# Optimization experiments

Hardware: AMD Instinct MI355X
Metric: run time of the kernel (lower is better)

## Reference

```python
import jax, jax.numpy as jnp
import numpy as np

NUM_CLASSES = 80
STRIDES = (8, 16, 32)
FEAT_HW = ((80, 80), (40, 40), (20, 20))
B = 32
MAX_GT = 60


def setup_inputs() -> dict:
    key = jax.random.key(0)
    ks = jax.random.split(key, 6)
    feats = {}
    for i, (s, (h, w)) in enumerate(zip(STRIDES, FEAT_HW)):
        feats[f"feat{s}"] = jax.random.normal(ks[i], (B, 5 + NUM_CLASSES, h, w), jnp.float32)
    u = jax.random.uniform(ks[3], (B, MAX_GT, 4), jnp.float32)
    # cx,cy in [0,640), w,h in [8,128): realistic pixel-space gt boxes for a 640x640 image
    gt_boxes = jnp.concatenate([u[..., :2] * 640.0, u[..., 2:] * 120.0 + 8.0], -1)
    gt_classes = jax.random.randint(ks[4], (B, MAX_GT), 0, NUM_CLASSES)
    num_gts = jax.random.randint(ks[5], (B,), 1, MAX_GT + 1)
    return dict(feat8=feats["feat8"], feat16=feats["feat16"], feat32=feats["feat32"],
                gt_boxes=gt_boxes, gt_classes=gt_classes, num_gts=num_gts)


def _decode(feat, stride):
    # torch get_output_and_grid: xy=(raw+grid)*stride, wh=exp(raw)*stride
    b, c, h, w = feat.shape
    yv, xv = jnp.meshgrid(jnp.arange(h), jnp.arange(w), indexing="ij")
    gx = xv.reshape(-1).astype(feat.dtype)  # [H*W]
    gy = yv.reshape(-1).astype(feat.dtype)
    out = feat.reshape(b, c, h * w).transpose(0, 2, 1)  # [B,A,C]
    xy = (out[..., :2] + jnp.stack([gx, gy], -1)[None]) * stride
    wh = jnp.exp(out[..., 2:4]) * stride
    return jnp.concatenate([xy, wh, out[..., 4:]], -1), gx, gy


def _pair_iou(a, b):
    # a: [G,4] xywh, b: [A,4] xywh -> [G,A] IoU (bboxes_iou, xyxy=False)
    tl = jnp.maximum(a[:, None, :2] - a[:, None, 2:] * 0.5, b[None, :, :2] - b[None, :, 2:] * 0.5)
    br = jnp.minimum(a[:, None, :2] + a[:, None, 2:] * 0.5, b[None, :, :2] + b[None, :, 2:] * 0.5)
    en = jnp.all(tl < br, -1)
    inter = jnp.where(en, jnp.prod(br - tl, -1), 0.0)
    area_a = jnp.prod(a[:, 2:], -1)
    area_b = jnp.prod(b[:, 2:], -1)
    return inter / (area_a[:, None] + area_b[None, :] - inter + 1e-16)


def _bce_logits(x, t):
    return jnp.maximum(x, 0.0) - x * t + jnp.log1p(jnp.exp(-jnp.abs(x)))


def _iou_loss(pred, tgt):
    # IOUloss(loss_type='iou'): 1 - iou^2, per box
    tl = jnp.maximum(pred[..., :2] - pred[..., 2:] * 0.5, tgt[..., :2] - tgt[..., 2:] * 0.5)
    br = jnp.minimum(pred[..., :2] + pred[..., 2:] * 0.5, tgt[..., :2] + tgt[..., 2:] * 0.5)
    en = jnp.all(tl < br, -1)
    inter = jnp.where(en, jnp.prod(br - tl, -1), 0.0)
    union = jnp.prod(pred[..., 2:], -1) + jnp.prod(tgt[..., 2:], -1) - inter
    iou = inter / (union + 1e-16)
    return 1.0 - iou ** 2


def _assign(boxes, cls_lo, obj_lo, gtb, gtc, vmask, cx, cy, st):
    # SimOTA per image. boxes [A,4], cls_lo [A,C], obj_lo [A], gtb [G,4], gtc [G] int,
    # vmask [G] bool (gt padding), cx/cy/st [A] anchor centers & strides.
    G, A = gtb.shape[0], boxes.shape[0]
    iou = _pair_iou(gtb, boxes)  # [G,A]
    gx, gy = gtb[:, :1], gtb[:, 1:2]
    gw, gh = gtb[:, 2:3], gtb[:, 3:4]
    in_box = ((cx[None] > gx - 0.5 * gw) & (cx[None] < gx + 0.5 * gw) &
              (cy[None] > gy - 0.5 * gh) & (cy[None] < gy + 0.5 * gh))
    R = 2.5  # center sampling radius (in strides)
    in_ctr = ((cx[None] > gx - R * st[None]) & (cx[None] < gx + R * st[None]) &
              (cy[None] > gy - R * st[None]) & (cy[None] < gy + R * st[None]))
    fg = ((in_box | in_ctr) & vmask[:, None]).any(0)  # [A] candidate anchors
    in_both = (in_box & in_ctr).astype(boxes.dtype)
    # pairwise cls cost: BCE(sqrt(sig(cls)*sig(obj)), onehot(gt_cls)).sum(-1),
    # decomposed to avoid the [G,A,C] tensor: sum_c bce0 + (bce1-bce0)[gt_cls]
    p = jnp.clip(jnp.sqrt(jax.nn.sigmoid(cls_lo) * jax.nn.sigmoid(obj_lo)[:, None]), 1e-7, 1.0 - 1e-7)
    bce1 = -jnp.log(p)          # [A,C]
    bce0 = -jnp.log(1.0 - p)    # [A,C]
    cls_cost = bce0.sum(-1)[None, :] + (bce1 - bce0)[:, gtc].T  # [G,A]
    cost = (cls_cost + 3.0 * (-jnp.log(iou + 1e-8))
            + 100000.0 * (1.0 - in_both)
            + 1e9 * (~fg)[None, :].astype(boxes.dtype)
            + 1e9 * (~vmask)[:, None].astype(boxes.dtype))
    K = 10  # n_candidate_k
    topk_ious, _ = jax.lax.top_k(iou * fg[None, :], K)
    dyn_k = jnp.maximum(topk_ious.sum(-1).astype(jnp.int32), 1)  # clamp(int(sum), min=1)
    _, pos = jax.lax.top_k(-cost, K)  # [G,K] lowest-cost anchors per gt
    sel = (jnp.arange(K)[None, :] < dyn_k[:, None]).astype(boxes.dtype)
    matching = jnp.zeros((G, A), boxes.dtype).at[jnp.arange(G)[:, None], pos].set(sel)
    matching = matching * vmask[:, None].astype(boxes.dtype)
    # resolve anchors claimed by >1 gt: keep min-cost gt
    conflict = matching.sum(0) > 1
    best_gt = jnp.argmin(cost, axis=0)  # [A]
    matching = jnp.where(conflict[None, :], jax.nn.one_hot(best_gt, G, dtype=matching.dtype).T, matching)
    fg_final = matching.sum(0) > 0  # [A]
    matched = jnp.argmax(matching, axis=0)  # [A]
    pred_iou = (matching * iou).sum(0)  # [A]
    cls_t = jax.nn.one_hot(gtc[matched], NUM_CLASSES, dtype=boxes.dtype) * pred_iou[:, None]
    reg_t = gtb[matched]
    return fg_final, cls_t, reg_t


def _forward(feat8, feat16, feat32, gt_boxes, gt_classes, num_gts):
    outs, cxs, cys, sts = [], [], [], []
    for f, s in zip((feat8, feat16, feat32), STRIDES):
        o, gx, gy = _decode(f, float(s))
        outs.append(o)
        cxs.append((gx + 0.5) * s)
        cys.append((gy + 0.5) * s)
        sts.append(jnp.full_like(gx, s))
    preds = jnp.concatenate(outs, 1)  # [B,A,5+C]
    cx = jnp.concatenate(cxs)
    cy = jnp.concatenate(cys)
    st = jnp.concatenate(sts)
    boxes = preds[..., :4]
    obj_lo = preds[..., 4]
    cls_lo = preds[..., 5:]
    vmask = jnp.arange(MAX_GT)[None, :] < num_gts[:, None]
    fg, cls_t, reg_t = jax.vmap(_assign, in_axes=(0, 0, 0, 0, 0, 0, None, None, None))(
        boxes, cls_lo, obj_lo, gt_boxes, gt_classes, vmask, cx, cy, st)
    # SimOTA assignment is no_grad in YOLOX: targets are constants wrt preds
    fg = jax.lax.stop_gradient(fg)
    cls_t = jax.lax.stop_gradient(cls_t)
    reg_t = jax.lax.stop_gradient(reg_t)
    fg_f = fg.astype(boxes.dtype)
    num_fg = jnp.maximum(fg_f.sum(), 1.0)
    loss_iou = (_iou_loss(boxes, reg_t) * fg_f).sum()
    loss_obj = _bce_logits(obj_lo, fg_f * 0.9).sum()  # obj_targets * 0.9 smoothing
    loss_cls = (_bce_logits(cls_lo, cls_t) * fg_f[..., None]).sum()
    REG_WEIGHT = 5.0
    return (REG_WEIGHT * loss_iou + loss_obj + loss_cls) / num_fg


def reference(feat8, feat16, feat32, gt_boxes, gt_classes, num_gts):
    return _forward(feat8, feat16, feat32, gt_boxes, gt_classes, num_gts)
```

## Files before the change

kernel.cpp:

```cpp
#include <hip/hip_runtime.h>

constexpr int kB = 32;
constexpr int kA = 8400;
constexpr int kG = 60;
constexpr int kC = 80;
constexpr int kK = 10;
constexpr int kNBx = (kA + 255)/256;
constexpr int kNB = kNBx * kB;

__device__ __forceinline__ float fexp(float x){ return __expf(x); }
__device__ __forceinline__ float flog(float x){ return __logf(x); }
__device__ __forceinline__ float frcp(float x){ return __builtin_amdgcn_rcpf(x); }
__device__ __forceinline__ float frsq(float x){ return __builtin_amdgcn_rsqf(x); }
__device__ __forceinline__ float fsqrt(float x){ return __builtin_amdgcn_sqrtf(x); }
__device__ __forceinline__ float fdiv(float a, float b){ return a * __builtin_amdgcn_rcpf(b); }
__device__ __forceinline__ float sigm(float x){ return frcp(1.0f + fexp(-x)); }
__device__ __forceinline__ float bce(float x, float t){
  return fmaxf(x, 0.0f) - x*t + flog(1.0f + fexp(-fabsf(x)));
}

__device__ __forceinline__ unsigned ordbits(float v){
  unsigned u = __float_as_uint(v);
  return (u & 0x80000000u) ? ~u : (u | 0x80000000u);
}
__device__ __forceinline__ float unpackf(unsigned k){
  return __uint_as_float((k & 0x80000000u) ? (k & 0x7fffffffu) : ~k);
}

struct AInfo { int x, y; float st; };
__device__ __forceinline__ AInfo ainfo(int a){
  AInfo r;
  if (a < 6400)      { r.x = a % 80;           r.y = a / 80;           r.st = 8.0f;  }
  else if (a < 8000) { int l = a-6400; r.x = l % 40; r.y = l / 40;     r.st = 16.0f; }
  else               { int l = a-8000; r.x = l % 20; r.y = l / 20;     r.st = 32.0f; }
  return r;
}

__device__ __forceinline__ float featv(const float* __restrict__ f8,
                                       const float* __restrict__ f16,
                                       const float* __restrict__ f32x,
                                       int b, int ch, int a){
  if (a < 6400) return f8 [(b*85 + ch)*6400 + a];
  if (a < 8000) return f16[(b*85 + ch)*1600 + (a - 6400)];
  return             f32x[(b*85 + ch)*400  + (a - 8000)];
}

__device__ __forceinline__ float pair_iou(float4 g, float4 p){
  float tlx = fmaxf(g.x - g.z*0.5f, p.x - p.z*0.5f);
  float tly = fmaxf(g.y - g.w*0.5f, p.y - p.w*0.5f);
  float brx = fminf(g.x + g.z*0.5f, p.x + p.z*0.5f);
  float bry = fminf(g.y + g.w*0.5f, p.y + p.w*0.5f);
  float inter = (tlx < brx && tly < bry) ? (brx-tlx)*(bry-tly) : 0.0f;
  return fdiv(inter, g.z*g.w + p.z*p.w - inter + 1e-16f);
}

__device__ __forceinline__ float cost_core(float iou, float cl, float obs, float b0sum,
                                           int a, float4 gt, int fg_a){
  AInfo ai = ainfo(a);
  float cx = ((float)ai.x + 0.5f)*ai.st;
  float cy = ((float)ai.y + 0.5f)*ai.st;
  bool in_box = (cx > gt.x - 0.5f*gt.z) && (cx < gt.x + 0.5f*gt.z)
             && (cy > gt.y - 0.5f*gt.w) && (cy < gt.y + 0.5f*gt.w);
  bool in_ctr = (cx > gt.x - 2.5f*ai.st) && (cx < gt.x + 2.5f*ai.st)
             && (cy > gt.y - 2.5f*ai.st) && (cy < gt.y + 2.5f*ai.st);
  float p = fsqrt(sigm(cl) * obs);
  p = fminf(fmaxf(p, 1e-7f), 1.0f - 1e-7f);
  float diff = -flog(p) + flog(1.0f - p);
  float c = b0sum + diff;
  c += 3.0f * (-flog(iou + 1e-8f));
  c += (in_box && in_ctr) ? 0.0f : 100000.0f;
  c += fg_a ? 0.0f : 1000000000.0f;
  return c;
}

__device__ __forceinline__ void insert10(unsigned long long* arr, unsigned long long key){
  if (key > arr[kK-1]){
    arr[kK-1] = key;
    #pragma unroll
    for (int i = kK-1; i > 0; --i)
      if (arr[i] > arr[i-1]){ unsigned long long t = arr[i]; arr[i] = arr[i-1]; arr[i-1] = t; }
  }
}

__global__ __launch_bounds__(256) void k_decode(
    const float* __restrict__ f8, const float* __restrict__ f16, const float* __restrict__ f32x,
    const float* __restrict__ gtb, const int* __restrict__ ngts,
    float* __restrict__ boxes, float* __restrict__ objl, float* __restrict__ b0s,
    float* __restrict__ bceS, float* __restrict__ obsA,
    int* __restrict__ fg, int* __restrict__ cnt, int* __restrict__ mtch){
  int b = blockIdx.y;
  int tid = threadIdx.x;
  int a = blockIdx.x*256 + tid;
  __shared__ float4 sg[kG];
  if (tid < kG) sg[tid] = ((const float4*)gtb)[b*kG + tid];
  __syncthreads();
  if (a >= kA) return;
  int ng = ngts[b];
  const float* base; int hw, off; float st_; int gx, gy;
  if (a < 6400)      { base=f8;   hw=6400; off=a;        st_=8.0f;  gx=off%80; gy=off/80; }
  else if (a < 8000) { base=f16;  hw=1600; off=a-6400;   st_=16.0f; gx=off%40; gy=off/40; }
  else               { base=f32x; hw=400;  off=a-8000;   st_=32.0f; gx=off%20; gy=off/20; }
  const float* p0 = base + ((size_t)b*85)*hw + off;
  float t0 = p0[0];
  float t1 = p0[(size_t)hw];
  float t2 = p0[(size_t)2*hw];
  float t3 = p0[(size_t)3*hw];
  float ob = p0[(size_t)4*hw];
  float4 bx;
  bx.x = (t0 + (float)gx) * st_;
  bx.y = (t1 + (float)gy) * st_;
  bx.z = fexp(t2) * st_;
  bx.w = fexp(t3) * st_;
  int idx = b*kA + a;
  ((float4*)boxes)[idx] = bx;
  objl[idx] = ob;
  float obs = sigm(ob);
  obsA[idx] = obs;
  float so = fsqrt(obs);
  float s = 0.0f;
  float sumCl = 0.0f;
  float slogv = 0.0f;
  const float* pc = p0 + (size_t)5*hw;
  #pragma unroll 2
  for (int grp = 0; grp < kC/8; ++grp){
    float prodS = 1.0f, prodV = 1.0f;
    #pragma unroll
    for (int j = 0; j < 8; ++j){
      float cl = pc[(size_t)(grp*8 + j)*hw];
      float u = fexp(-cl);
      float v = 1.0f + u;
      float p = so * frsq(v);
      p = fminf(fmaxf(p, 1e-7f), 1.0f - 1e-7f);
      prodS *= (1.0f - p);
      prodV *= v;
      sumCl += cl;
    }
    s -= flog(prodS);
    slogv += flog(prodV);
  }
  b0s[idx] = s;
  bceS[idx] = sumCl + slogv;
  float cx = ((float)gx + 0.5f)*st_;
  float cy = ((float)gy + 0.5f)*st_;
  int f = 0;
  for (int g = 0; g < ng; ++g){
    float4 gt = sg[g];
    bool in_box = (cx > gt.x - 0.5f*gt.z) && (cx < gt.x + 0.5f*gt.z)
               && (cy > gt.y - 0.5f*gt.w) && (cy < gt.y + 0.5f*gt.w);
    bool in_ctr = (cx > gt.x - 2.5f*st_) && (cx < gt.x + 2.5f*st_)
               && (cy > gt.y - 2.5f*st_) && (cy < gt.y + 2.5f*st_);
    if (in_box || in_ctr){ f = 1; break; }
  }
  fg[idx] = f;
  cnt[idx] = 0;
  mtch[idx] = 0x7fffffff;
}

__global__ __launch_bounds__(1024) void k_compact(
    const int* __restrict__ fg, unsigned short* __restrict__ alist, int* __restrict__ mcnt){
  int b = blockIdx.x;
  int tid = threadIdx.x;
  const int CH = 9;
  int start = tid*CH;
  int myf[CH]; int cl = 0;
  #pragma unroll
  for (int j = 0; j < CH; ++j){
    int a = start + j;
    int f = (a < kA) ? fg[b*kA + a] : 0;
    myf[j] = f; cl += f;
  }
  __shared__ int s1[1024], s2[1024];
  int* cur = s1; int* nxt = s2;
  cur[tid] = cl; __syncthreads();
  for (int off = 1; off < 1024; off <<= 1){
    int v = cur[tid];
    if (tid >= off) v += cur[tid - off];
    nxt[tid] = v; __syncthreads();
    int* t = cur; cur = nxt; nxt = t;
  }
  int o = cur[tid] - cl;
  unsigned short* out = alist + (size_t)b*kA;
  #pragma unroll
  for (int j = 0; j < CH; ++j){
    int a = start + j;
    if (a < kA && myf[j]) out[o++] = (unsigned short)a;
  }
  if (tid == 1023) mcnt[b] = cur[tid];
}

__global__ __launch_bounds__(256) void k_assign(
    const float* __restrict__ f8, const float* __restrict__ f16, const float* __restrict__ f32x,
    const float* __restrict__ gtb, const int* __restrict__ gtc, const int* __restrict__ ngts,
    const float* __restrict__ boxes, const float* __restrict__ obsA, const float* __restrict__ b0s,
    const int* __restrict__ fg, const unsigned short* __restrict__ alist, const int* __restrict__ mcnt,
    int* __restrict__ cnt, int* __restrict__ mtch){
  int b = blockIdx.x / kG;
  int g = blockIdx.x % kG;
  if (g >= ngts[b]) return;
  int tid = threadIdx.x;
  int lane = tid & 63, wid = tid >> 6;
  float4 gt = ((const float4*)gtb)[b*kG + g];
  int cls = gtc[b*kG + g];
  const float4* bx4 = (const float4*)boxes;
  const float* c8  = f8   + ((size_t)b*85 + 5 + cls)*6400;
  const float* c16 = f16  + ((size_t)b*85 + 5 + cls)*1600;
  const float* c32 = f32x + ((size_t)b*85 + 5 + cls)*400;
  int m = mcnt[b];
  bool full0 = (m < kK);
  int len = full0 ? kA : m;
  const unsigned short* al = alist + (size_t)b*kA;

  __shared__ unsigned long long stop1[4][kK], stop2[4][kK];
  __shared__ int swb[4];

  unsigned long long k1[kK], k2[kK];
  #pragma unroll
  for (int i = 0; i < kK; ++i){ k1[i] = 0ull; k2[i] = 0ull; }
  int nboth = 0;

  for (int i = tid; i < len; i += 256){
    int a = full0 ? i : (int)al[i];
    int idx = b*kA + a;
    float4 bx = bx4[idx];
    float iou = pair_iou(gt, bx);
    if (full0){
      int fga = fg[idx];
      float v = fga ? iou : 0.0f;
      insert10(k1, ((unsigned long long)ordbits(v) << 32) | (unsigned)(~a));
      float cl = (a < 6400) ? c8[a] : (a < 8000) ? c16[a-6400] : c32[a-8000];
      float c = cost_core(iou, cl, obsA[idx], b0s[idx], a, gt, fga);
      insert10(k2, ~(((unsigned long long)ordbits(c) << 32) | (unsigned)a));
    } else {
      insert10(k1, ((unsigned long long)ordbits(iou) << 32) | (unsigned)(~a));
      AInfo ai = ainfo(a);
      float cx = ((float)ai.x + 0.5f)*ai.st;
      float cy = ((float)ai.y + 0.5f)*ai.st;
      bool in_box = (cx > gt.x - 0.5f*gt.z) && (cx < gt.x + 0.5f*gt.z)
                 && (cy > gt.y - 0.5f*gt.w) && (cy < gt.y + 0.5f*gt.w);
      bool in_ctr = (cx > gt.x - 2.5f*ai.st) && (cx < gt.x + 2.5f*ai.st)
                 && (cy > gt.y - 2.5f*ai.st) && (cy < gt.y + 2.5f*ai.st);
      if (in_box && in_ctr){
        ++nboth;
        float cl = (a < 6400) ? c8[a] : (a < 8000) ? c16[a-6400] : c32[a-8000];
        float c = cost_core(iou, cl, obsA[idx], b0s[idx], a, gt, 1);
        insert10(k2, ~(((unsigned long long)ordbits(c) << 32) | (unsigned)a));
      }
    }
  }

  int nb = nboth;
  #pragma unroll
  for (int off = 32; off; off >>= 1) nb += __shfl_down(nb, off, 64);
  if (lane == 0) swb[wid] = nb;
  __syncthreads();
  int sboth = swb[0] + swb[1] + swb[2] + swb[3];

  if (!full0 && sboth < kK){
    #pragma unroll
    for (int i = 0; i < kK; ++i) k2[i] = 0ull;
    for (int i = tid; i < len; i += 256){
      int a = (int)al[i];
      int idx = b*kA + a;
      float iou = pair_iou(gt, bx4[idx]);
      float cl = (a < 6400) ? c8[a] : (a < 8000) ? c16[a-6400] : c32[a-8000];
      float c = cost_core(iou, cl, obsA[idx], b0s[idx], a, gt, 1);
      insert10(k2, ~(((unsigned long long)ordbits(c) << 32) | (unsigned)a));
    }
  }

  #pragma unroll 1
  for (int k = 0; k < kK; ++k){
    unsigned long long best = k1[0];
    #pragma unroll
    for (int off = 32; off; off >>= 1){
      unsigned long long o = __shfl_xor(best, off, 64);
      if (o > best) best = o;
    }
    if (k1[0] == best){
      #pragma unroll
      for (int i = 0; i < kK-1; ++i) k1[i] = k1[i+1];
      k1[kK-1] = 0ull;
    }
    if (lane == 0) stop1[wid][k] = best;
  }
  #pragma unroll 1
  for (int k = 0; k < kK; ++k){
    unsigned long long best = k2[0];
    #pragma unroll
    for (int off = 32; off; off >>= 1){
      unsigned long long o = __shfl_xor(best, off, 64);
      if (o > best) best = o;
    }
    if (k2[0] == best){
      #pragma unroll
      for (int i = 0; i < kK-1; ++i) k2[i] = k2[i+1];
      k2[kK-1] = 0ull;
    }
    if (lane == 0) stop2[wid][k] = best;
  }
  __syncthreads();

  if (wid == 0){
    unsigned long long cand1 = (lane < 40) ? stop1[lane/kK][lane % kK] : 0ull;
    unsigned long long cand2 = (lane < 40) ? stop2[lane/kK][lane % kK] : 0ull;
    float ksum = 0.0f;
    #pragma unroll 1
    for (int k = 0; k < kK; ++k){
      unsigned long long best = cand1;
      #pragma unroll
      for (int off = 32; off; off >>= 1){
        unsigned long long o = __shfl_xor(best, off, 64);
        if (o > best) best = o;
      }
      if (cand1 == best) cand1 = 0ull;
      ksum += unpackf((unsigned)(best >> 32));
    }
    int dynk = max((int)ksum, 1);
    int my_a = -1;
    #pragma unroll 1
    for (int k = 0; k < kK; ++k){
      unsigned long long best = cand2;
      #pragma unroll
      for (int off = 32; off; off >>= 1){
        unsigned long long o = __shfl_xor(best, off, 64);
        if (o > best) best = o;
      }
      if (cand2 == best) cand2 = 0ull;
      if (lane == k) my_a = (int)((unsigned)(~best) & 0xffffffffu);
    }
    if (lane < kK && lane < dynk){
      atomicAdd(&cnt[b*kA + my_a], 1);
      atomicMin(&mtch[b*kA + my_a], g);
    }
  }
}

__global__ __launch_bounds__(256) void k_loss(
    const float* __restrict__ f8, const float* __restrict__ f16, const float* __restrict__ f32x,
    const float* __restrict__ gtb, const int* __restrict__ gtc, const int* __restrict__ ngts,
    const float* __restrict__ boxes, const float* __restrict__ objl, const float* __restrict__ b0s,
    const float* __restrict__ bceS, const float* __restrict__ obsA,
    const int* __restrict__ fg, const int* __restrict__ cnt, const int* __restrict__ mtch,
    float4* __restrict__ pacc){
  int b = blockIdx.y;
  int a = blockIdx.x*256 + threadIdx.x;
  int tid = threadIdx.x;
  __shared__ float4 sg[kG];
  __shared__ int scls[kG];
  if (tid < kG){ sg[tid] = ((const float4*)gtb)[b*kG + tid]; scls[tid] = gtc[b*kG + tid]; }
  __syncthreads();
  float li = 0.0f, lo = 0.0f, lc = 0.0f, nf = 0.0f;
  bool valid = (a < kA);
  int idx = valid ? (b*kA + a) : (b*kA);
  int c = valid ? cnt[idx] : 0;
  float ob = valid ? objl[idx] : 0.0f;
  float4 bx = valid ? ((const float4*)boxes)[idx] : make_float4(0,0,1,1);

  float fgf = 0.0f; int mg = 0;
  if (valid && c == 1){ mg = mtch[idx]; fgf = 1.0f; }
  bool need = valid && (c > 1);
  if (__any(need)){
    if (need){
      int ng = ngts[b];
      float b0 = b0s[idx];
      float obs = obsA[idx];
      int fga = fg[idx];
      float bestc = 3.0e38f; int bg = 0;
      for (int g = 0; g < ng; ++g){
        float iou = pair_iou(sg[g], bx);
        float cl = featv(f8,f16,f32x,b,5+scls[g],a);
        float cst = cost_core(iou, cl, obs, b0, a, sg[g], fga);
        if (cst < bestc){ bestc = cst; bg = g; }
      }
      mg = bg; fgf = 1.0f;
    }
  }
  if (valid){
    lo = bce(ob, fgf*0.9f);
    if (fgf > 0.0f){
      nf = 1.0f;
      float4 r = sg[mg];
      float piou = pair_iou(r, bx);
      float tlx = fmaxf(bx.x - bx.z*0.5f, r.x - r.z*0.5f);
      float tly = fmaxf(bx.y - bx.w*0.5f, r.y - r.w*0.5f);
      float brx = fminf(bx.x + bx.z*0.5f, r.x + r.z*0.5f);
      float bry = fminf(bx.y + bx.w*0.5f, r.y + r.w*0.5f);
      float inter = (tlx < brx && tly < bry) ? (brx-tlx)*(bry-tly) : 0.0f;
      float un = bx.z*bx.w + r.z*r.w - inter;
      float iou = fdiv(inter, un + 1e-16f);
      li = 1.0f - iou*iou;
      int tc = scls[mg];
      float cl_tc = featv(f8,f16,f32x,b,5+tc,a);
      lc = bceS[idx] - piou * cl_tc;
    }
  }
  for (int off = 32; off > 0; off >>= 1){
    li += __shfl_down(li, off, 64);
    lo += __shfl_down(lo, off, 64);
    lc += __shfl_down(lc, off, 64);
    nf += __shfl_down(nf, off, 64);
  }
  __shared__ float4 wred[4];
  int wid = tid >> 6;
  if ((tid & 63) == 0) wred[wid] = make_float4(li, lo, lc, nf);
  __syncthreads();
  if (tid == 0){
    float4 t = wred[0];
    for (int w = 1; w < 4; ++w){
      float4 o = wred[w];
      t.x += o.x; t.y += o.y; t.z += o.z; t.w += o.w;
    }
    pacc[blockIdx.y * gridDim.x + blockIdx.x] = t;
  }
}

__global__ __launch_bounds__(256) void k_final(
    const float4* __restrict__ pacc, float* __restrict__ out){
  int tid = threadIdx.x;
  float li = 0.0f, lo = 0.0f, lc = 0.0f, nf = 0.0f;
  for (int i = tid; i < kNB; i += 256){
    float4 p = pacc[i];
    li += p.x; lo += p.y; lc += p.z; nf += p.w;
  }
  for (int off = 32; off > 0; off >>= 1){
    li += __shfl_down(li, off, 64);
    lo += __shfl_down(lo, off, 64);
    lc += __shfl_down(lc, off, 64);
    nf += __shfl_down(nf, off, 64);
  }
  __shared__ float4 wred[4];
  int wid = tid >> 6;
  if ((tid & 63) == 0) wred[wid] = make_float4(li, lo, lc, nf);
  __syncthreads();
  if (tid == 0){
    float4 t = wred[0];
    for (int w = 1; w < 4; ++w){
      float4 o = wred[w];
      t.x += o.x; t.y += o.y; t.z += o.z; t.w += o.w;
    }
    out[0] = (5.0f*t.x + t.y + t.z) * frcp(fmaxf(t.w, 1.0f));
  }
}

extern "C" void kernel_launch(void* const* d_in, const int* in_sizes, int n_in,
                              void* d_out, int out_size, void* d_ws, size_t ws_size,
                              hipStream_t stream) {
  (void)in_sizes; (void)n_in; (void)out_size; (void)ws_size;
  const float* f8   = (const float*)d_in[0];
  const float* f16  = (const float*)d_in[1];
  const float* f32x = (const float*)d_in[2];
  const float* gtb  = (const float*)d_in[3];
  const int*   gtc  = (const int*)d_in[4];
  const int*   ngts = (const int*)d_in[5];
  float* out = (float*)d_out;

  const size_t BA = (size_t)kB*kA;
  float* ws    = (float*)d_ws;
  float* boxes = ws;
  float* objl  = boxes + BA*4;
  float* b0s   = objl  + BA;
  float* bceS  = b0s   + BA;
  float* obsA  = bceS  + BA;
  int*   fg    = (int*)(obsA + BA);
  int*   cnt   = fg  + BA;
  int*   mtch  = cnt + BA;
  unsigned short* alist = (unsigned short*)(mtch + BA);
  int*   mcnt  = (int*)(alist + BA);
  float4* pacc = (float4*)(mcnt + kB);

  dim3 gBA(kNBx, kB);
  k_decode<<<gBA, dim3(256), 0, stream>>>(f8,f16,f32x,gtb,ngts,boxes,objl,b0s,bceS,obsA,fg,cnt,mtch);
  k_compact<<<dim3(kB), dim3(1024), 0, stream>>>(fg, alist, mcnt);
  k_assign<<<dim3(kB*kG), dim3(256), 0, stream>>>(f8,f16,f32x,gtb,gtc,ngts,boxes,obsA,b0s,fg,alist,mcnt,cnt,mtch);
  k_loss<<<gBA, dim3(256), 0, stream>>>(f8,f16,f32x,gtb,gtc,ngts,boxes,objl,b0s,bceS,obsA,fg,cnt,mtch,pacc);
  k_final<<<dim3(1), dim3(256), 0, stream>>>(pacc, out);
}
```

Baseline: 223.2 us.

## Replace per-thread top-10 heaps in SimOTA assign with shared-memory candidate compaction and rank selection

The assign kernel no longer keeps per-thread top-10 insertion lists followed by multi-stage wave reductions. It compacts positive-IoU values and in-box-and-center candidates into shared memory with ballot and atomic offsets, then picks the top-k by counting ranks. The fg==0 full-scan path is dropped, which assumes the compacted list always covers the needed candidates. The compaction kernel also moves from a 1024-thread shared-memory scan to 256 threads with a wave shuffle scan and bitmasks. Fixed capacities (2048 and 128) risk silently truncating candidates, and the quadratic rank loops could cost more when the candidate count is large.

```diff
diff --git a/kernel.cpp b/kernel.cpp
--- a/kernel.cpp
+++ b/kernel.cpp
@@ -7,6 +7,8 @@
 constexpr int kK = 10;
 constexpr int kNBx = (kA + 255)/256;
 constexpr int kNB = kNBx * kB;
+constexpr int kCap1 = 2048;
+constexpr int kCap2 = 128;
 
 __device__ __forceinline__ float fexp(float x){ return __expf(x); }
 __device__ __forceinline__ float flog(float x){ return __logf(x); }
@@ -80,6 +82,15 @@
     for (int i = kK-1; i > 0; --i)
       if (arr[i] > arr[i-1]){ unsigned long long t = arr[i]; arr[i] = arr[i-1]; arr[i-1] = t; }
   }
+}
+
+__device__ __forceinline__ unsigned long long wave_max64(unsigned long long v){
+  #pragma unroll
+  for (int off = 32; off; off >>= 1){
+    unsigned long long o = __shfl_xor(v, off, 64);
+    if (o > v) v = o;
+  }
+  return v;
 }
 
 __global__ __launch_bounds__(256) void k_decode(
@@ -117,9 +128,7 @@
   float obs = sigm(ob);
   obsA[idx] = obs;
   float so = fsqrt(obs);
-  float s = 0.0f;
-  float sumCl = 0.0f;
-  float slogv = 0.0f;
+  float s = 0.0f, sumCl = 0.0f, slogv = 0.0f;
   const float* pc = p0 + (size_t)5*hw;
   #pragma unroll 2
   for (int grp = 0; grp < kC/8; ++grp){
@@ -156,43 +165,47 @@
   mtch[idx] = 0x7fffffff;
 }
 
-__global__ __launch_bounds__(1024) void k_compact(
+__global__ __launch_bounds__(256) void k_compact(
     const int* __restrict__ fg, unsigned short* __restrict__ alist, int* __restrict__ mcnt){
   int b = blockIdx.x;
   int tid = threadIdx.x;
-  const int CH = 9;
+  int lane = tid & 63, wid = tid >> 6;
+  const int CH = 33;
   int start = tid*CH;
-  int myf[CH]; int cl = 0;
+  unsigned long long bits = 0ull;
+  int cl = 0;
   #pragma unroll
   for (int j = 0; j < CH; ++j){
     int a = start + j;
     int f = (a < kA) ? fg[b*kA + a] : 0;
-    myf[j] = f; cl += f;
-  }
-  __shared__ int s1[1024], s2[1024];
-  int* cur = s1; int* nxt = s2;
-  cur[tid] = cl; __syncthreads();
-  for (int off = 1; off < 1024; off <<= 1){
-    int v = cur[tid];
-    if (tid >= off) v += cur[tid - off];
-    nxt[tid] = v; __syncthreads();
-    int* t = cur; cur = nxt; nxt = t;
-  }
-  int o = cur[tid] - cl;
+    bits |= ((unsigned long long)(f & 1)) << j;
+    cl += f;
+  }
+  int incl = cl;
+  #pragma unroll
+  for (int off = 1; off < 64; off <<= 1){
+    int o = __shfl_up(incl, off, 64);
+    if (lane >= off) incl += o;
+  }
+  __shared__ int swt[4];
+  if (lane == 63) swt[wid] = incl;
+  __syncthreads();
+  int base = 0;
+  for (int w = 0; w < 4; ++w) if (w < wid) base += swt[w];
+  int o = base + incl - cl;
   unsigned short* out = alist + (size_t)b*kA;
-  #pragma unroll
+  #pragma unroll 1
   for (int j = 0; j < CH; ++j){
-    int a = start + j;
-    if (a < kA && myf[j]) out[o++] = (unsigned short)a;
-  }
-  if (tid == 1023) mcnt[b] = cur[tid];
+    if ((bits >> j) & 1ull) out[o++] = (unsigned short)(start + j);
+  }
+  if (tid == 0) mcnt[b] = swt[0] + swt[1] + swt[2] + swt[3];
 }
 
 __global__ __launch_bounds__(256) void k_assign(
     const float* __restrict__ f8, const float* __restrict__ f16, const float* __restrict__ f32x,
     const float* __restrict__ gtb, const int* __restrict__ gtc, const int* __restrict__ ngts,
     const float* __restrict__ boxes, const float* __restrict__ obsA, const float* __restrict__ b0s,
-    const int* __restrict__ fg, const unsigned short* __restrict__ alist, const int* __restrict__ mcnt,
+    const unsigned short* __restrict__ alist, const int* __restrict__ mcnt,
     int* __restrict__ cnt, int* __restrict__ mtch){
   int b = blockIdx.x / kG;
   int g = blockIdx.x % kG;
@@ -206,32 +219,108 @@
   const float* c16 = f16  + ((size_t)b*85 + 5 + cls)*1600;
   const float* c32 = f32x + ((size_t)b*85 + 5 + cls)*400;
   int m = mcnt[b];
-  bool full0 = (m < kK);
-  int len = full0 ? kA : m;
+  bool pushAll = (m < kK);
   const unsigned short* al = alist + (size_t)b*kA;
 
-  __shared__ unsigned long long stop1[4][kK], stop2[4][kK];
-  __shared__ int swb[4];
-
-  unsigned long long k1[kK], k2[kK];
-  #pragma unroll
-  for (int i = 0; i < kK; ++i){ k1[i] = 0ull; k2[i] = 0ull; }
-  int nboth = 0;
-
-  for (int i = tid; i < len; i += 256){
-    int a = full0 ? i : (int)al[i];
+  __shared__ unsigned p1v[kCap1];
+  __shared__ unsigned long long p2k[kCap2];
+  __shared__ int sn1, sn2, sdynk;
+  __shared__ float sred[4];
+  __shared__ unsigned long long stop[4][kK];
+  if (tid == 0){ sn1 = 0; sn2 = 0; }
+  __syncthreads();
+
+  for (int i = tid; i < m; i += 256){
+    int a = (int)al[i];
     int idx = b*kA + a;
     float4 bx = bx4[idx];
     float iou = pair_iou(gt, bx);
-    if (full0){
-      int fga = fg[idx];
-      float v = fga ? iou : 0.0f;
-      insert10(k1, ((unsigned long long)ordbits(v) << 32) | (unsigned)(~a));
-      float cl = (a < 6400) ? c8[a] : (a < 8000) ? c16[a-6400] : c32[a-8000];
-      float c = cost_core(iou, cl, obsA[idx], b0s[idx], a, gt, fga);
-      insert10(k2, ~(((unsigned long long)ordbits(c) << 32) | (unsigned)a));
-    } else {
-      insert10(k1, ((unsigned long long)ordbits(iou) << 32) | (unsigned)(~a));
+    bool pos = (iou > 0.0f);
+    unsigned long long bm = __ballot(pos);
+    if (bm){
+      int wb = 0;
+      if (lane == 0) wb = atomicAdd(&sn1, (int)__popcll(bm));
+      wb = __shfl(wb, 0, 64);
+      if (pos){
+        int off = wb + (int)__popcll(bm & ((1ull << lane) - 1ull));
+        if (off < kCap1) p1v[off] = ordbits(iou);
+      }
+    }
+    AInfo ai = ainfo(a);
+    float cx = ((float)ai.x + 0.5f)*ai.st;
+    float cy = ((float)ai.y + 0.5f)*ai.st;
+    bool in_box = (cx > gt.x - 0.5f*gt.z) && (cx < gt.x + 0.5f*gt.z)
+               && (cy > gt.y - 0.5f*gt.w) && (cy < gt.y + 0.5f*gt.w);
+    bool in_ctr = (cx > gt.x - 2.5f*ai.st) && (cx < gt.x + 2.5f*ai.st)
+               && (cy > gt.y - 2.5f*ai.st) && (cy < gt.y + 2.5f*ai.st);
+    bool p2c = pushAll || (in_box && in_ctr);
+    unsigned long long bm2 = __ballot(p2c);
+    if (bm2){
+      int wb2 = 0;
+      if (lane == 0) wb2 = atomicAdd(&sn2, (int)__popcll(bm2));
+      wb2 = __shfl(wb2, 0, 64);
+      if (p2c){
+        float cl = (a < 6400) ? c8[a] : (a < 8000) ? c16[a-6400] : c32[a-8000];
+        float c = cost_core(iou, cl, obsA[idx], b0s[idx], a, gt, 1);
+        int off = wb2 + (int)__popcll(bm2 & ((1ull << lane) - 1ull));
+        if (off < kCap2) p2k[off] = ~(((unsigned long long)ordbits(c) << 32) | (unsigned)a);
+      }
+    }
+  }
+  __syncthreads();
+  int n1 = min(sn1, kCap1);
+  int n2 = min(sn2, kCap2);
+
+  float part = 0.0f;
+  if (n1 <= kK){
+    for (int i = tid; i < n1; i += 256) part += unpackf(p1v[i]);
+  } else {
+    for (int i = tid; i < n1; i += 256){
+      unsigned v = p1v[i];
+      int r = 0;
+      for (int j = 0; j < n1; ++j){
+        unsigned w = p1v[j];
+        r += (int)((w > v) || (w == v && j < i));
+        if (r >= kK) break;
+      }
+      if (r < kK) part += unpackf(v);
+    }
+  }
+  #pragma unroll
+  for (int off = 32; off; off >>= 1) part += __shfl_down(part, off, 64);
+  if (lane == 0) sred[wid] = part;
+  __syncthreads();
+  if (tid == 0){
+    float s = sred[0] + sred[1] + sred[2] + sred[3];
+    sdynk = max((int)s, 1);
+  }
+  __syncthreads();
+  int dynk = sdynk;
+
+  if (n2 >= dynk){
+    for (int i = tid; i < n2; i += 256){
+      unsigned long long k = p2k[i];
+      int r = 0;
+      for (int j = 0; j < n2; ++j) r += (int)(p2k[j] > k);
+      if (r < dynk){
+        int a = (int)((unsigned)(~k));
+        atomicAdd(&cnt[b*kA + a], 1);
+        atomicMin(&mtch[b*kA + a], g);
+      }
+    }
+  } else {
+    for (int i = tid; i < n2; i += 256){
+      int a = (int)((unsigned)(~p2k[i]));
+      atomicAdd(&cnt[b*kA + a], 1);
+      atomicMin(&mtch[b*kA + a], g);
+    }
+    unsigned long long kept[kK];
+    #pragma unroll
+    for (int i = 0; i < kK; ++i) kept[i] = 0ull;
+    for (int i = tid; i < m; i += 256){
+      int a = (int)al[i];
+      int idx = b*kA + a;
+      float4 bx = bx4[idx];
       AInfo ai = ainfo(a);
       float cx = ((float)ai.x + 0.5f)*ai.st;
       float cy = ((float)ai.y + 0.5f)*ai.st;
@@ -239,98 +328,38 @@
                  && (cy > gt.y - 0.5f*gt.w) && (cy < gt.y + 0.5f*gt.w);
       bool in_ctr = (cx > gt.x - 2.5f*ai.st) && (cx < gt.x + 2.5f*ai.st)
                  && (cy > gt.y - 2.5f*ai.st) && (cy < gt.y + 2.5f*ai.st);
-      if (in_box && in_ctr){
-        ++nboth;
+      if (!(in_box && in_ctr)){
+        float iou = pair_iou(gt, bx);
         float cl = (a < 6400) ? c8[a] : (a < 8000) ? c16[a-6400] : c32[a-8000];
         float c = cost_core(iou, cl, obsA[idx], b0s[idx], a, gt, 1);
-        insert10(k2, ~(((unsigned long long)ordbits(c) << 32) | (unsigned)a));
-      }
-    }
-  }
-
-  int nb = nboth;
-  #pragma unroll
-  for (int off = 32; off; off >>= 1) nb += __shfl_down(nb, off, 64);
-  if (lane == 0) swb[wid] = nb;
-  __syncthreads();
-  int sboth = swb[0] + swb[1] + swb[2] + swb[3];
-
-  if (!full0 && sboth < kK){
-    #pragma unroll
-    for (int i = 0; i < kK; ++i) k2[i] = 0ull;
-    for (int i = tid; i < len; i += 256){
-      int a = (int)al[i];
-      int idx = b*kA + a;
-      float iou = pair_iou(gt, bx4[idx]);
-      float cl = (a < 6400) ? c8[a] : (a < 8000) ? c16[a-6400] : c32[a-8000];
-      float c = cost_core(iou, cl, obsA[idx], b0s[idx], a, gt, 1);
-      insert10(k2, ~(((unsigned long long)ordbits(c) << 32) | (unsigned)a));
-    }
-  }
-
-  #pragma unroll 1
-  for (int k = 0; k < kK; ++k){
-    unsigned long long best = k1[0];
-    #pragma unroll
-    for (int off = 32; off; off >>= 1){
-      unsigned long long o = __shfl_xor(best, off, 64);
-      if (o > best) best = o;
-    }
-    if (k1[0] == best){
-      #pragma unroll
-      for (int i = 0; i < kK-1; ++i) k1[i] = k1[i+1];
-      k1[kK-1] = 0ull;
-    }
-    if (lane == 0) stop1[wid][k] = best;
-  }
-  #pragma unroll 1
-  for (int k = 0; k < kK; ++k){
-    unsigned long long best = k2[0];
-    #pragma unroll
-    for (int off = 32; off; off >>= 1){
-      unsigned long long o = __shfl_xor(best, off, 64);
-      if (o > best) best = o;
-    }
-    if (k2[0] == best){
-      #pragma unroll
-      for (int i = 0; i < kK-1; ++i) k2[i] = k2[i+1];
-      k2[kK-1] = 0ull;
-    }
-    if (lane == 0) stop2[wid][k] = best;
-  }
-  __syncthreads();
-
-  if (wid == 0){
-    unsigned long long cand1 = (lane < 40) ? stop1[lane/kK][lane % kK] : 0ull;
-    unsigned long long cand2 = (lane < 40) ? stop2[lane/kK][lane % kK] : 0ull;
-    float ksum = 0.0f;
+        insert10(kept, ~(((unsigned long long)ordbits(c) << 32) | (unsigned)a));
+      }
+    }
     #pragma unroll 1
     for (int k = 0; k < kK; ++k){
-      unsigned long long best = cand1;
-      #pragma unroll
-      for (int off = 32; off; off >>= 1){
-        unsigned long long o = __shfl_xor(best, off, 64);
-        if (o > best) best = o;
-      }
-      if (cand1 == best) cand1 = 0ull;
-      ksum += unpackf((unsigned)(best >> 32));
-    }
-    int dynk = max((int)ksum, 1);
-    int my_a = -1;
-    #pragma unroll 1
-    for (int k = 0; k < kK; ++k){
-      unsigned long long best = cand2;
-      #pragma unroll
-      for (int off = 32; off; off >>= 1){
-        unsigned long long o = __shfl_xor(best, off, 64);
-        if (o > best) best = o;
-      }
-      if (cand2 == best) cand2 = 0ull;
-      if (lane == k) my_a = (int)((unsigned)(~best) & 0xffffffffu);
-    }
-    if (lane < kK && lane < dynk){
-      atomicAdd(&cnt[b*kA + my_a], 1);
-      atomicMin(&mtch[b*kA + my_a], g);
+      unsigned long long best = wave_max64(kept[0]);
+      if (kept[0] == best && best){
+        #pragma unroll
+        for (int i = 0; i < kK-1; ++i) kept[i] = kept[i+1];
+        kept[kK-1] = 0ull;
+      }
+      if (lane == 0) stop[wid][k] = best;
+    }
+    __syncthreads();
+    if (wid == 0){
+      unsigned long long cand = (lane < 4*kK) ? stop[lane/kK][lane % kK] : 0ull;
+      int need = dynk - n2;
+      #pragma unroll 1
+      for (int k = 0; k < kK; ++k){
+        if (k >= need) break;
+        unsigned long long best = wave_max64(cand);
+        if (cand == best) cand = 0ull;
+        if (lane == 0 && best){
+          int a = (int)((unsigned)(~best));
+          atomicAdd(&cnt[b*kA + a], 1);
+          atomicMin(&mtch[b*kA + a], g);
+        }
+      }
     }
   }
 }
@@ -394,6 +423,7 @@
       lc = bceS[idx] - piou * cl_tc;
     }
   }
+  #pragma unroll
   for (int off = 32; off > 0; off >>= 1){
     li += __shfl_down(li, off, 64);
     lo += __shfl_down(lo, off, 64);
@@ -422,6 +452,7 @@
     float4 p = pacc[i];
     li += p.x; lo += p.y; lc += p.z; nf += p.w;
   }
+  #pragma unroll
   for (int off = 32; off > 0; off >>= 1){
     li += __shfl_down(li, off, 64);
     lo += __shfl_down(lo, off, 64);
@@ -470,8 +501,8 @@
 
   dim3 gBA(kNBx, kB);
   k_decode<<<gBA, dim3(256), 0, stream>>>(f8,f16,f32x,gtb,ngts,boxes,objl,b0s,bceS,obsA,fg,cnt,mtch);
-  k_compact<<<dim3(kB), dim3(1024), 0, stream>>>(fg, alist, mcnt);
-  k_assign<<<dim3(kB*kG), dim3(256), 0, stream>>>(f8,f16,f32x,gtb,gtc,ngts,boxes,obsA,b0s,fg,alist,mcnt,cnt,mtch);
+  k_compact<<<dim3(kB), dim3(256), 0, stream>>>(fg, alist, mcnt);
+  k_assign<<<dim3(kB*kG), dim3(256), 0, stream>>>(f8,f16,f32x,gtb,gtc,ngts,boxes,obsA,b0s,alist,mcnt,cnt,mtch);
   k_loss<<<gBA, dim3(256), 0, stream>>>(f8,f16,f32x,gtb,gtc,ngts,boxes,objl,b0s,bceS,obsA,fg,cnt,mtch,pacc);
   k_final<<<dim3(1), dim3(256), 0, stream>>>(pacc, out);
 }
```

Measured after the change: 260.6 us. +16.8%, slower.
